# Performance work log

Hardware: AMD Instinct MI355X
Metric: run time of the kernel (lower is better)

Reference implementation:

```python
import jax, jax.numpy as jnp
import numpy as np

B, S, D, U = 32, 2048, 1024, 1024


def setup_inputs() -> dict:
    key = jax.random.key(0)
    ks = jax.random.split(key, 10)
    s = 0.02
    return {
        "dec_hidden": jax.random.normal(ks[0], (B, D), jnp.float32),
        "enc_output": jax.random.normal(ks[1], (B, S, D), jnp.float32),
        "enc_pad_mask": jnp.ones((B, S), jnp.int32),  # accepted but unused, as in the original
        "use_coverage": True,
        "prev_coverage": jax.random.uniform(ks[2], (B, S, 1), jnp.float32),
        "Ws_w": jax.random.normal(ks[3], (D, U), jnp.float32) * s,
        "Ws_b": jnp.zeros((U,), jnp.float32),
        "Wh_w": jax.random.normal(ks[4], (D, U), jnp.float32) * s,
        "Wh_b": jnp.zeros((U,), jnp.float32),
        "Wc_w": jax.random.normal(ks[5], (1, U), jnp.float32) * s,
        "Wc_b": jnp.zeros((U,), jnp.float32),
        "V_w": jax.random.normal(ks[6], (U, 1), jnp.float32) * s,
        "V_b": jnp.zeros((1,), jnp.float32),
    }


def reference(dec_hidden, enc_output, enc_pad_mask, use_coverage, prev_coverage,
              Ws_w, Ws_b, Wh_w, Wh_b, Wc_w, Wc_b, V_w, V_b):
    # W_h(dec_hidden) with time axis: [B, 1, U]
    h = (dec_hidden @ Wh_w + Wh_b)[:, None, :]
    # W_s(enc_output): [B, S, U]
    feat = jnp.einsum('bsd,du->bsu', enc_output, Ws_w) + Ws_b + h
    if use_coverage and prev_coverage is not None:
        # W_c(prev_coverage): [B, S, 1] @ [1, U] -> [B, S, U]
        feat = feat + prev_coverage @ Wc_w + Wc_b
        score = jnp.tanh(feat) @ V_w + V_b            # [B, S, 1]
        attention_weights = jax.nn.softmax(score, axis=1)
        coverage = attention_weights + prev_coverage
    else:
        score = jnp.tanh(feat) @ V_w + V_b
        attention_weights = jax.nn.softmax(score, axis=1)
        coverage = attention_weights if use_coverage else []
    # weighted sum over sequence axis: [B, D]
    context_vector = jnp.sum(attention_weights * enc_output, axis=1)
    return context_vector, jnp.squeeze(attention_weights, -1), coverage
```

## Files before the change

### kernel.cpp

```cpp
#include <hip/hip_runtime.h>
#include <hip/hip_bf16.h>

namespace {

constexpr int kB = 32;
constexpr int kS = 2048;
constexpr int kD = 1024;
constexpr int kU = 1024;

constexpr int BM = 256;
constexpr int BN = 256;
constexpr int kKT = kD / 64;
constexpr int kMT = (kB * kS) / BM;
constexpr int kNT = kU / BN;
constexpr size_t kHalf = 16384;
constexpr size_t kTileChunk = 2 * kHalf;
constexpr size_t kPanel = (size_t)kKT * kTileChunk;

constexpr int kConvBlocks = (kB * kS * kD / 8) / 256;
constexpr int kTpBlocks = (kU / 32) * (kD / 32);
constexpr int kH2Blocks = (kU / 64) * (kB / 4);
constexpr int kPrepBlocks = kConvBlocks + kTpBlocks + kH2Blocks;

typedef __attribute__((ext_vector_type(8))) short bf16x8;
typedef __attribute__((ext_vector_type(4))) float f32x4;

__device__ __forceinline__ unsigned short f2bf(float x) {
  union { __hip_bfloat16 h; unsigned short u; } c;
  c.h = __float2bfloat16(x);
  return c.u;
}

__device__ __forceinline__ float bf2f(unsigned short u) {
  union { unsigned int i; float f; } c;
  c.i = ((unsigned int)u) << 16;
  return c.f;
}

__device__ __forceinline__ float tanh_fast(float x) {
  float e = __expf(2.0f * x);
  return 1.0f - 2.0f * __builtin_amdgcn_rcpf(e + 1.0f);
}

__device__ __forceinline__ void gload16(const void* g, void* l) {
  __builtin_amdgcn_global_load_lds(
      (const __attribute__((address_space(1))) void*)g,
      (__attribute__((address_space(3))) void*)l, 16, 0, 0);
}

#define MFMA_BF16(a, b, c) __builtin_amdgcn_mfma_f32_16x16x32_bf16((a), (b), (c), 0, 0, 0)


__global__ __launch_bounds__(256) void prep_kernel(
    const float* __restrict__ enc, unsigned char* __restrict__ encT,
    const float* __restrict__ Wsw, unsigned char* __restrict__ Bt,
    const float* __restrict__ dec, const float* __restrict__ Whw,
    const float* __restrict__ Whb, const float* __restrict__ Wsb,
    const float* __restrict__ Wcb, float* __restrict__ h2) {
  __shared__ float tile[32][33];
  const int bid = blockIdx.x;
  if (bid < kConvBlocks) {
    const size_t e = ((size_t)bid * 256 + threadIdx.x) * 8;
    const int r = (int)(e >> 10), d0 = (int)(e & 1023);
    float4 v0 = *(const float4*)(enc + e);
    float4 v1 = *(const float4*)(enc + e + 4);
    uint4 p;
    p.x = (unsigned)f2bf(v0.x) | ((unsigned)f2bf(v0.y) << 16);
    p.y = (unsigned)f2bf(v0.z) | ((unsigned)f2bf(v0.w) << 16);
    p.z = (unsigned)f2bf(v1.x) | ((unsigned)f2bf(v1.y) << 16);
    p.w = (unsigned)f2bf(v1.z) | ((unsigned)f2bf(v1.w) << 16);
    const int mt = r >> 8, rh = (r >> 7) & 1, row = r & 127;
    const int kt = d0 >> 6, c8 = (d0 & 63) >> 3;
    unsigned char* dst = encT + (size_t)mt * kPanel + (size_t)kt * kTileChunk +
                         (size_t)rh * kHalf + row * 128 +
                         (((unsigned)c8 << 4) ^ (((unsigned)row & 7) << 4));
    *(uint4*)dst = p;
  } else if (bid < kConvBlocks + kTpBlocks) {
    const int q = bid - kConvBlocks;
    const int u0 = (q & 31) * 32, d0 = (q >> 5) * 32;
    const int tx = threadIdx.x & 31, ty = threadIdx.x >> 5;
    #pragma unroll
    for (int i = 0; i < 4; ++i)
      tile[ty + i * 8][tx] = Wsw[(size_t)(d0 + ty + i * 8) * kU + u0 + tx];
    __syncthreads();
    #pragma unroll
    for (int i = 0; i < 4; ++i) {
      const int u = u0 + ty + i * 8, d = d0 + tx;
      const int nt = u >> 8, gh = (u >> 7) & 1, n = u & 127;
      const int kt = d >> 6, c = d & 63;
      *(unsigned short*)(Bt + (size_t)nt * kPanel + (size_t)kt * kTileChunk +
                         (size_t)gh * kHalf + n * 128 +
                         (((((unsigned)c >> 3) << 4) ^ (((unsigned)n & 7) << 4)) +
                          (c & 7) * 2)) = f2bf(tile[tx][ty + i * 8]);
    }
  } else {
    const int q = bid - kConvBlocks - kTpBlocks;
    const int u = (q & 15) * 64 + (threadIdx.x & 63);
    const int b = (q >> 4) * 4 + (threadIdx.x >> 6);
    float acc = 0.f;
    const float* dh = dec + b * kD;
    #pragma unroll 8
    for (int d = 0; d < kD; ++d) acc += dh[d] * Whw[(size_t)d * kU + u];
    h2[b * kU + u] = acc + Whb[u] + Wsb[u] + Wcb[u];
  }
}

#define READ_A8(AF, ABASE, QR)                                                 \
  _Pragma("unroll")                                                            \
  for (int rfl = 0; rfl < 4; ++rfl) {                                          \
    _Pragma("unroll")                                                          \
    for (int ks = 0; ks < 2; ++ks) {                                           \
      const int row_ = ((QR)*4 + rfl) * 16 + lr;                               \
      AF[rfl][ks] = *(const bf16x8*)((ABASE) + row_ * 128 +                    \
                                     ((ks * 64 + lq * 16) ^ ((lr & 7) << 4))); \
    }                                                                          \
  }

#define READ_B4(BF, BBASE, QC)                                                 \
  _Pragma("unroll")                                                            \
  for (int cfl = 0; cfl < 2; ++cfl) {                                          \
    _Pragma("unroll")                                                          \
    for (int ks = 0; ks < 2; ++ks) {                                           \
      const int row_ = ((QC)*2 + cfl) * 16 + lr;                               \
      BF[cfl][ks] = *(const bf16x8*)((BBASE) + row_ * 128 +                    \
                                     ((ks * 64 + lq * 16) ^ ((lr & 7) << 4))); \
    }                                                                          \
  }

#define MF16(QR, QC, AF, BF)                                                   \
  _Pragma("unroll")                                                            \
  for (int ks = 0; ks < 2; ++ks) {                                             \
    _Pragma("unroll")                                                          \
    for (int rfl = 0; rfl < 4; ++rfl) {                                        \
      _Pragma("unroll")                                                        \
      for (int cfl = 0; cfl < 2; ++cfl)                                        \
        acc[(QR)*4 + rfl][(QC)*2 + cfl] =                                      \
            MFMA_BF16(AF[rfl][ks], BF[cfl][ks], acc[(QR)*4 + rfl][(QC)*2 + cfl]); \
    }                                                                          \
  }

#define STAGE2(GSRC, LDST)                                                     \
  gload16((GSRC) + so0, (LDST) + so0);                                         \
  gload16((GSRC) + so1, (LDST) + so1);

#define FENCE asm volatile("" ::: "memory")
#define BARRIER { FENCE; __builtin_amdgcn_s_barrier(); FENCE; }

__global__ __launch_bounds__(512, 1) void score_gemm4_kernel(
    const unsigned char* __restrict__ encT, const unsigned char* __restrict__ Bt,
    const float* __restrict__ h2, const float* __restrict__ pc,
    const float* __restrict__ Wcw, const float* __restrict__ Vw,
    float* __restrict__ scorep) {
  __shared__ __attribute__((aligned(16))) unsigned char lds[131072];

  const int tid = threadIdx.x;
  const int lane = tid & 63;
  const int w = tid >> 6;
  const int lr = lane & 15, lq = lane >> 4;
  const int wm = w >> 2;
  const int wn = w & 3;
  const int g = wn >> 1;

  const int work = (blockIdx.x & 7) * 128 + (blockIdx.x >> 3);
  const int mtile = work >> 2, ntile = work & 3;

  const unsigned char* Ab = encT + (size_t)mtile * kPanel;
  const unsigned char* Bb = Bt + (size_t)ntile * kPanel;
  const int so0 = tid * 16;
  const int so1 = tid * 16 + 8192;

  unsigned char* Ad0 = lds + (size_t)wm * kHalf;
  unsigned char* Ad1 = lds + (2 + wm) * kHalf;
  unsigned char* Bd0 = lds + 65536 + (size_t)g * kHalf + (wn & 1) * 8192;
  unsigned char* Bd1 = lds + 65536 + (2 + g) * kHalf + (wn & 1) * 8192;
  unsigned char* aSlot[2][2] = {{lds, lds + kHalf}, {lds + 2 * kHalf, lds + 3 * kHalf}};
  unsigned char* bSlot[2][2] = {{lds + 65536, lds + 65536 + kHalf},
                                {lds + 65536 + 2 * kHalf, lds + 65536 + 3 * kHalf}};

  f32x4 acc[8][4];
  #pragma unroll
  for (int i = 0; i < 8; ++i)
    #pragma unroll
    for (int j = 0; j < 4; ++j) acc[i][j] = (f32x4){0.f, 0.f, 0.f, 0.f};

  bf16x8 af[4][2], b0[2][2], b1[2][2];

  STAGE2(Bb, bSlot[0][0]);
  STAGE2(Bb + kHalf, bSlot[0][1]);
  STAGE2(Ab, aSlot[0][0]);
  STAGE2(Ab + kHalf, aSlot[0][1]);
  STAGE2(Bb + kTileChunk, bSlot[1][0]);
  STAGE2(Bb + kTileChunk + kHalf, bSlot[1][1]);
  asm volatile("s_waitcnt vmcnt(4)" ::: "memory");
  BARRIER;

  for (int i = 0; i < kKT / 2; ++i) {
    const int t2 = (i < kKT / 2 - 1) ? 2 * i + 2 : 2 * i;
    const int t3 = (i < kKT / 2 - 1) ? 2 * i + 3 : 2 * i;
    const unsigned char* sA1 = Ab + (size_t)(2 * i + 1) * kTileChunk;
    const unsigned char* sA2 = Ab + (size_t)t2 * kTileChunk;
    const unsigned char* sB2 = Bb + (size_t)t2 * kTileChunk;
    const unsigned char* sB3 = Bb + (size_t)t3 * kTileChunk;

    READ_A8(af, Ad0, 0);
    READ_B4(b0, Bd0, 0);
    STAGE2(sA1, aSlot[1][0]);
    BARRIER;
    __builtin_amdgcn_s_setprio(1);
    MF16(0, 0, af, b0);
    __builtin_amdgcn_s_setprio(0);
    BARRIER;

    READ_B4(b1, Bd0, 1);
    STAGE2(sA1 + kHalf, aSlot[1][1]);
    BARRIER;
    __builtin_amdgcn_s_setprio(1);
    MF16(0, 1, af, b1);
    __builtin_amdgcn_s_setprio(0);
    BARRIER;

    READ_A8(af, Ad0, 1);
    STAGE2(sB2, bSlot[0][0]);
    BARRIER;
    __builtin_amdgcn_s_setprio(1);
    MF16(1, 0, af, b0);
    __builtin_amdgcn_s_setprio(0);
    BARRIER;

    STAGE2(sB2 + kHalf, bSlot[0][1]);
    asm volatile("s_waitcnt vmcnt(4)" ::: "memory");
    BARRIER;
    __builtin_amdgcn_s_setprio(1);
    MF16(1, 1, af, b1);
    __builtin_amdgcn_s_setprio(0);
    BARRIER;

    READ_A8(af, Ad1, 0);
    READ_B4(b0, Bd1, 0);
    STAGE2(sA2, aSlot[0][0]);
    BARRIER;
    __builtin_amdgcn_s_setprio(1);
    MF16(0, 0, af, b0);
    __builtin_amdgcn_s_setprio(0);
    BARRIER;

    READ_B4(b1, Bd1, 1);
    STAGE2(sA2 + kHalf, aSlot[0][1]);
    BARRIER;
    __builtin_amdgcn_s_setprio(1);
    MF16(0, 1, af, b1);
    __builtin_amdgcn_s_setprio(0);
    BARRIER;

    READ_A8(af, Ad1, 1);
    STAGE2(sB3, bSlot[1][0]);
    BARRIER;
    __builtin_amdgcn_s_setprio(1);
    MF16(1, 0, af, b0);
    __builtin_amdgcn_s_setprio(0);
    BARRIER;

    STAGE2(sB3 + kHalf, bSlot[1][1]);
    asm volatile("s_waitcnt vmcnt(4)" ::: "memory");
    BARRIER;
    __builtin_amdgcn_s_setprio(1);
    MF16(1, 1, af, b1);
    __builtin_amdgcn_s_setprio(0);
    BARRIER;
  }
  asm volatile("s_waitcnt vmcnt(0)" ::: "memory");

  const int bidx = mtile >> 3;
  float hv[4], wv[4], vv[4];
  #pragma unroll
  for (int cf = 0; cf < 4; ++cf) {
    const int u = ntile * BN + wn * 64 + cf * 16 + lr;
    hv[cf] = h2[bidx * kU + u];
    wv[cf] = Wcw[u];
    vv[cf] = Vw[u];
  }
  float* plane = scorep + (size_t)(ntile * 4 + wn) * (kB * kS);
  #pragma unroll
  for (int rf = 0; rf < 8; ++rf) {
    #pragma unroll
    for (int j = 0; j < 4; ++j) {
      const int r = mtile * BM + wm * 128 + rf * 16 + lq * 4 + j;
      const float pcv = pc[r];
      float partial = 0.f;
      #pragma unroll
      for (int cf = 0; cf < 4; ++cf) {
        const float feat = acc[rf][cf][j] + hv[cf] + pcv * wv[cf];
        partial += tanh_fast(feat) * vv[cf];
      }
      partial += __shfl_xor(partial, 1);
      partial += __shfl_xor(partial, 2);
      partial += __shfl_xor(partial, 4);
      partial += __shfl_xor(partial, 8);
      if (lr == 0) plane[r] = partial;
    }
  }
}

__global__ __launch_bounds__(256) void softmax2_kernel(
    const float* __restrict__ scorep, const float* __restrict__ pc,
    float* __restrict__ attn, float* __restrict__ cov) {
  const int b = blockIdx.x, tid = threadIdx.x;
  const int lane = tid & 63, wid = tid >> 6;
  const size_t base = (size_t)b * kS + tid * 8;
  float v[8] = {0.f, 0.f, 0.f, 0.f, 0.f, 0.f, 0.f, 0.f};
  #pragma unroll
  for (int p = 0; p < 16; ++p) {
    const float* s = scorep + (size_t)p * (kB * kS) + base;
    float4 a = *(const float4*)(s);
    float4 c = *(const float4*)(s + 4);
    v[0] += a.x; v[1] += a.y; v[2] += a.z; v[3] += a.w;
    v[4] += c.x; v[5] += c.y; v[6] += c.z; v[7] += c.w;
  }
  float m = v[0];
  #pragma unroll
  for (int i = 1; i < 8; ++i) m = fmaxf(m, v[i]);
  #pragma unroll
  for (int msk = 1; msk < 64; msk <<= 1) m = fmaxf(m, __shfl_xor(m, msk));
  __shared__ float redm[4], reds[4];
  if (lane == 0) redm[wid] = m;
  __syncthreads();
  m = fmaxf(fmaxf(redm[0], redm[1]), fmaxf(redm[2], redm[3]));
  float e[8], sum = 0.f;
  #pragma unroll
  for (int i = 0; i < 8; ++i) { e[i] = __expf(v[i] - m); sum += e[i]; }
  #pragma unroll
  for (int msk = 1; msk < 64; msk <<= 1) sum += __shfl_xor(sum, msk);
  if (lane == 0) reds[wid] = sum;
  __syncthreads();
  sum = reds[0] + reds[1] + reds[2] + reds[3];
  const float inv = 1.0f / sum;
  float pv[8], a[8], c[8];
  const float* p = pc + base;
  *(float4*)(pv) = *(const float4*)(p);
  *(float4*)(pv + 4) = *(const float4*)(p + 4);
  #pragma unroll
  for (int i = 0; i < 8; ++i) { a[i] = e[i] * inv; c[i] = a[i] + pv[i]; }
  *(float4*)(attn + base) = *(float4*)(a);
  *(float4*)(attn + base + 4) = *(float4*)(a + 4);
  *(float4*)(cov + base) = *(float4*)(c);
  *(float4*)(cov + base + 4) = *(float4*)(c + 4);
}

__global__ __launch_bounds__(256) void context2_kernel(
    const unsigned char* __restrict__ encT, const float* __restrict__ attn,
    float* __restrict__ ctx) {
  const int kt = blockIdx.x;
  const int b = blockIdx.y;
  const int cg = threadIdx.x & 7;
  const int rgrp = threadIdx.x >> 3;
  float acc8[8];
  #pragma unroll
  for (int j = 0; j < 8; ++j) acc8[j] = 0.f;
  const float* ab = attn + (size_t)b * kS;
  for (int it = 0; it < kS / 32; ++it) {
    const int s = it * 32 + rgrp;
    const int r = b * kS + s;
    const int mt = r >> 8, rh = (r >> 7) & 1, row = r & 127;
    const unsigned char* chunk = encT + (size_t)mt * kPanel +
                                 (size_t)kt * kTileChunk + (size_t)rh * kHalf;
    uint4 v = *(const uint4*)(chunk + row * 128 +
                              ((((unsigned)cg << 4) ^ (((unsigned)row & 7) << 4))));
    const float a = ab[s];
    const unsigned int* vw = (const unsigned int*)&v;
    #pragma unroll
    for (int q = 0; q < 4; ++q) {
      acc8[2 * q]     += a * bf2f((unsigned short)(vw[q] & 0xffff));
      acc8[2 * q + 1] += a * bf2f((unsigned short)(vw[q] >> 16));
    }
  }
  __shared__ float red[256 * 8];
  #pragma unroll
  for (int j = 0; j < 8; ++j) red[threadIdx.x * 8 + j] = acc8[j];
  __syncthreads();
  for (int stride = 16; stride > 0; stride >>= 1) {
    if (rgrp < stride) {
      #pragma unroll
      for (int j = 0; j < 8; ++j)
        red[(rgrp * 8 + cg) * 8 + j] += red[((rgrp + stride) * 8 + cg) * 8 + j];
    }
    __syncthreads();
  }
  if (rgrp == 0) {
    #pragma unroll
    for (int j = 0; j < 8; ++j)
      ctx[(size_t)b * kD + kt * 64 + cg * 8 + j] = red[cg * 8 + j];
  }
}


__global__ __launch_bounds__(256) void h2b_kernel(
    const float* __restrict__ dec, const float* __restrict__ Whw,
    const float* __restrict__ Whb, const float* __restrict__ Wsb,
    const float* __restrict__ Wcb, float* __restrict__ h2) {
  const int u = blockIdx.x * 64 + (threadIdx.x & 63);
  const int b = blockIdx.y * 4 + (threadIdx.x >> 6);
  float acc = 0.f;
  const float* dh = dec + b * kD;
  #pragma unroll 8
  for (int d = 0; d < kD; ++d) acc += dh[d] * Whw[(size_t)d * kU + u];
  h2[b * kU + u] = acc + Whb[u] + Wsb[u] + Wcb[u];
}

__global__ __launch_bounds__(256) void tpose_fb_kernel(
    const float* __restrict__ W, unsigned short* __restrict__ out) {
  __shared__ float tile[32][33];
  const int u0 = blockIdx.x * 32, d0 = blockIdx.y * 32;
  const int tx = threadIdx.x & 31, ty = threadIdx.x >> 5;
  #pragma unroll
  for (int i = 0; i < 4; ++i)
    tile[ty + i * 8][tx] = W[(size_t)(d0 + ty + i * 8) * kU + u0 + tx];
  __syncthreads();
  #pragma unroll
  for (int i = 0; i < 4; ++i)
    out[(size_t)(u0 + ty + i * 8) * kD + d0 + tx] = f2bf(tile[tx][ty + i * 8]);
}

__global__ __launch_bounds__(256, 2) void score_gemm_fb_kernel(
    const float* __restrict__ enc, const unsigned short* __restrict__ WsT,
    const float* __restrict__ h2, const float* __restrict__ pc,
    const float* __restrict__ Wcw, const float* __restrict__ Vw,
    float* __restrict__ score) {
  __shared__ __attribute__((aligned(16))) unsigned char smA[128 * 64 * 2];
  __shared__ __attribute__((aligned(16))) unsigned char smB[128 * 64 * 2];
  const int tid = threadIdx.x;
  const int lane = tid & 63;
  const int wid = tid >> 6;
  const int wr = wid >> 1, wc = wid & 1;
  const int mtile = blockIdx.x >> 3, ntile = blockIdx.x & 7;
  const int r0 = mtile * 128, n0 = ntile * 128;
  f32x4 acc[4][4];
  #pragma unroll
  for (int i = 0; i < 4; ++i)
    #pragma unroll
    for (int j = 0; j < 4; ++j) acc[i][j] = (f32x4){0.f, 0.f, 0.f, 0.f};
  const int kqA = tid & 15;
  const int rowA = tid >> 4;
  const int kcB = tid & 7;
  const int nB = tid >> 3;
  float4 aReg[8];
  uint4 bReg[4];
  #pragma unroll
  for (int i = 0; i < 8; ++i)
    aReg[i] = *(const float4*)(enc + (size_t)(r0 + rowA + 16 * i) * kD + kqA * 4);
  #pragma unroll
  for (int i = 0; i < 4; ++i)
    bReg[i] = *(const uint4*)(WsT + (size_t)(n0 + nB + 32 * i) * kD + kcB * 8);
  const int lr = lane & 15, lq = lane >> 4;
  for (int k0 = 0; k0 < kD; k0 += 64) {
    #pragma unroll
    for (int i = 0; i < 8; ++i) {
      const int row = rowA + 16 * i;
      uint2 p;
      p.x = (unsigned)f2bf(aReg[i].x) | ((unsigned)f2bf(aReg[i].y) << 16);
      p.y = (unsigned)f2bf(aReg[i].z) | ((unsigned)f2bf(aReg[i].w) << 16);
      *(uint2*)(smA + row * 128 + ((kqA * 8) ^ ((row & 7) << 4))) = p;
    }
    #pragma unroll
    for (int i = 0; i < 4; ++i) {
      const int n = nB + 32 * i;
      *(uint4*)(smB + n * 128 + ((kcB * 16) ^ ((n & 7) << 4))) = bReg[i];
    }
    __syncthreads();
    if (k0 + 64 < kD) {
      const int kn = k0 + 64;
      #pragma unroll
      for (int i = 0; i < 8; ++i)
        aReg[i] = *(const float4*)(enc + (size_t)(r0 + rowA + 16 * i) * kD + kn + kqA * 4);
      #pragma unroll
      for (int i = 0; i < 4; ++i)
        bReg[i] = *(const uint4*)(WsT + (size_t)(n0 + nB + 32 * i) * kD + kn + kcB * 8);
    }
    #pragma unroll
    for (int ks = 0; ks < 2; ++ks) {
      const int kb = ks * 64 + lq * 16;
      bf16x8 af2[4], bfr[4];
      #pragma unroll
      for (int fm = 0; fm < 4; ++fm) {
        const int row = wr * 64 + fm * 16 + lr;
        af2[fm] = *(const bf16x8*)(smA + row * 128 + (kb ^ ((row & 7) << 4)));
      }
      #pragma unroll
      for (int fn = 0; fn < 4; ++fn) {
        const int n = wc * 64 + fn * 16 + lr;
        bfr[fn] = *(const bf16x8*)(smB + n * 128 + (kb ^ ((n & 7) << 4)));
      }
      #pragma unroll
      for (int fm = 0; fm < 4; ++fm)
        #pragma unroll
        for (int fn = 0; fn < 4; ++fn)
          acc[fm][fn] = MFMA_BF16(af2[fm], bfr[fn], acc[fm][fn]);
    }
    __syncthreads();
  }
  const int bidx = r0 >> 11;
  float hv[4], wv[4], vv[4];
  #pragma unroll
  for (int fn = 0; fn < 4; ++fn) {
    const int u = n0 + wc * 64 + fn * 16 + lr;
    hv[fn] = h2[bidx * kU + u];
    wv[fn] = Wcw[u];
    vv[fn] = Vw[u];
  }
  #pragma unroll
  for (int fm = 0; fm < 4; ++fm) {
    #pragma unroll
    for (int j = 0; j < 4; ++j) {
      const int r = r0 + wr * 64 + fm * 16 + lq * 4 + j;
      const float pcv = pc[r];
      float partial = 0.f;
      #pragma unroll
      for (int fn = 0; fn < 4; ++fn) {
        const float feat = acc[fm][fn][j] + hv[fn] + pcv * wv[fn];
        partial += tanh_fast(feat) * vv[fn];
      }
      partial += __shfl_xor(partial, 1);
      partial += __shfl_xor(partial, 2);
      partial += __shfl_xor(partial, 4);
      partial += __shfl_xor(partial, 8);
      if (lr == 0) atomicAdd(&score[r], partial);
    }
  }
}

__global__ __launch_bounds__(256) void softmax_fb_kernel(
    const float* __restrict__ score, const float* __restrict__ pc,
    float* __restrict__ attn, float* __restrict__ cov) {
  const int b = blockIdx.x, tid = threadIdx.x;
  const int lane = tid & 63, wid = tid >> 6;
  const float* s = score + (size_t)b * kS;
  float v[8];
  *(float4*)(v) = *(const float4*)(s + tid * 8);
  *(float4*)(v + 4) = *(const float4*)(s + tid * 8 + 4);
  float m = v[0];
  #pragma unroll
  for (int i = 1; i < 8; ++i) m = fmaxf(m, v[i]);
  #pragma unroll
  for (int msk = 1; msk < 64; msk <<= 1) m = fmaxf(m, __shfl_xor(m, msk));
  __shared__ float redm[4], reds[4];
  if (lane == 0) redm[wid] = m;
  __syncthreads();
  m = fmaxf(fmaxf(redm[0], redm[1]), fmaxf(redm[2], redm[3]));
  float e[8], sum = 0.f;
  #pragma unroll
  for (int i = 0; i < 8; ++i) { e[i] = __expf(v[i] - m); sum += e[i]; }
  #pragma unroll
  for (int msk = 1; msk < 64; msk <<= 1) sum += __shfl_xor(sum, msk);
  if (lane == 0) reds[wid] = sum;
  __syncthreads();
  sum = reds[0] + reds[1] + reds[2] + reds[3];
  const float inv = 1.0f / sum;
  float pv[8], a[8], c[8];
  const float* p = pc + (size_t)b * kS + tid * 8;
  *(float4*)(pv) = *(const float4*)(p);
  *(float4*)(pv + 4) = *(const float4*)(p + 4);
  #pragma unroll
  for (int i = 0; i < 8; ++i) { a[i] = e[i] * inv; c[i] = a[i] + pv[i]; }
  *(float4*)(attn + (size_t)b * kS + tid * 8) = *(float4*)(a);
  *(float4*)(attn + (size_t)b * kS + tid * 8 + 4) = *(float4*)(a + 4);
  *(float4*)(cov + (size_t)b * kS + tid * 8) = *(float4*)(c);
  *(float4*)(cov + (size_t)b * kS + tid * 8 + 4) = *(float4*)(c + 4);
}

__global__ __launch_bounds__(256) void context_fb_kernel(
    const float* __restrict__ enc, const float* __restrict__ attn,
    float* __restrict__ ctx) {
  const int b = blockIdx.z;
  const int s0 = blockIdx.y * 256;
  const int d = blockIdx.x * 256 + threadIdx.x;
  const float* e = enc + ((size_t)b * kS + s0) * kD + d;
  const float* a = attn + (size_t)b * kS + s0;
  float acc = 0.f;
  #pragma unroll 8
  for (int s = 0; s < 256; ++s) acc += a[s] * e[(size_t)s * kD];
  atomicAdd(&ctx[b * kD + d], acc);
}

}

extern "C" void kernel_launch(void* const* d_in, const int* in_sizes, int n_in,
                              void* d_out, int out_size, void* d_ws, size_t ws_size,
                              hipStream_t stream) {
  (void)in_sizes; (void)n_in; (void)out_size;
  const float* dec = (const float*)d_in[0];
  const float* enc = (const float*)d_in[1];
  const float* pc  = (const float*)d_in[4];
  const float* Wsw = (const float*)d_in[5];
  const float* Wsb = (const float*)d_in[6];
  const float* Whw = (const float*)d_in[7];
  const float* Whb = (const float*)d_in[8];
  const float* Wcw = (const float*)d_in[9];
  const float* Wcb = (const float*)d_in[10];
  const float* Vw  = (const float*)d_in[11];

  float* ctx  = (float*)d_out;
  float* attn = (float*)d_out + kB * kD;
  float* cov  = attn + kB * kS;

  unsigned char* ws = (unsigned char*)d_ws;

  const size_t encT_sz = (size_t)kB * kS * kD * 2;
  const size_t Bt_sz   = (size_t)kU * kD * 2;
  const size_t h2_sz   = (size_t)kB * kU * 4;
  const size_t sp_sz   = (size_t)16 * kB * kS * 4;
  const size_t need    = encT_sz + Bt_sz + h2_sz + sp_sz;

  if (ws_size >= need) {
    unsigned char* encT = ws;
    unsigned char* Bt   = ws + encT_sz;
    float* h2     = (float*)(ws + encT_sz + Bt_sz);
    float* scorep = (float*)(ws + encT_sz + Bt_sz + h2_sz);

    prep_kernel<<<dim3(kPrepBlocks), 256, 0, stream>>>(
        enc, encT, Wsw, Bt, dec, Whw, Whb, Wsb, Wcb, h2);
    score_gemm4_kernel<<<dim3(kMT * kNT), 512, 0, stream>>>(
        encT, Bt, h2, pc, Wcw, Vw, scorep);
    softmax2_kernel<<<dim3(kB), 256, 0, stream>>>(scorep, pc, attn, cov);
    context2_kernel<<<dim3(kD / 64, kB), 256, 0, stream>>>(encT, attn, ctx);
  } else {
    unsigned short* WsT = (unsigned short*)ws;
    float* h2    = (float*)(ws + (size_t)2 * 1024 * 1024);
    float* score = (float*)(ws + (size_t)2 * 1024 * 1024 + 131072);
    hipMemsetAsync(score, 0, kB * kS * sizeof(float), stream);
    hipMemsetAsync(ctx, 0, kB * kD * sizeof(float), stream);
    h2b_kernel<<<dim3(kU / 64, kB / 4), 256, 0, stream>>>(dec, Whw, Whb, Wsb, Wcb, h2);
    tpose_fb_kernel<<<dim3(kU / 32, kD / 32), 256, 0, stream>>>(Wsw, WsT);
    score_gemm_fb_kernel<<<dim3(4096), 256, 0, stream>>>(
        enc, WsT, h2, pc, Wcw, Vw, score);
    softmax_fb_kernel<<<dim3(kB), 256, 0, stream>>>(score, pc, attn, cov);
    context_fb_kernel<<<dim3(kD / 256, kS / 256, kB), 256, 0, stream>>>(enc, attn, ctx);
  }
}
```

Baseline: 309.7 us.

## Store bf16 encoder in row-major layout and swizzle on GEMM load

The prep kernel now writes the bf16 copy of enc_output in plain row-major order instead of a tiled, pre-swizzled panel layout. It also reorders prep blocks so the h2 and weight-transpose work is dispatched first. The GEMM's A-tile staging computes per-thread row-major source addresses and applies the XOR swizzle on the fly via the global-to-LDS loads. The context kernel reads rows contiguously. The intent is fully coalesced conversion writes and simpler context reads, at the cost of strided 16-byte global reads per row in the GEMM A loads.

```diff
diff --git a/kernel.cpp b/kernel.cpp
--- a/kernel.cpp
+++ b/kernel.cpp
@@ -17,10 +17,10 @@
 constexpr size_t kTileChunk = 2 * kHalf;
 constexpr size_t kPanel = (size_t)kKT * kTileChunk;
 
+constexpr int kH2Blocks = (kU / 64) * (kB / 4);
+constexpr int kTpBlocks = (kU / 32) * (kD / 32);
 constexpr int kConvBlocks = (kB * kS * kD / 8) / 256;
-constexpr int kTpBlocks = (kU / 32) * (kD / 32);
-constexpr int kH2Blocks = (kU / 64) * (kB / 4);
-constexpr int kPrepBlocks = kConvBlocks + kTpBlocks + kH2Blocks;
+constexpr int kPrepBlocks = kH2Blocks + kTpBlocks + kConvBlocks;
 
 typedef __attribute__((ext_vector_type(8))) short bf16x8;
 typedef __attribute__((ext_vector_type(4))) float f32x4;
@@ -52,33 +52,26 @@
 
 
 __global__ __launch_bounds__(256) void prep_kernel(
-    const float* __restrict__ enc, unsigned char* __restrict__ encT,
+    const float* __restrict__ enc, unsigned char* __restrict__ encR,
     const float* __restrict__ Wsw, unsigned char* __restrict__ Bt,
     const float* __restrict__ dec, const float* __restrict__ Whw,
     const float* __restrict__ Whb, const float* __restrict__ Wsb,
     const float* __restrict__ Wcb, float* __restrict__ h2) {
   __shared__ float tile[32][33];
   const int bid = blockIdx.x;
-  if (bid < kConvBlocks) {
-    const size_t e = ((size_t)bid * 256 + threadIdx.x) * 8;
-    const int r = (int)(e >> 10), d0 = (int)(e & 1023);
-    float4 v0 = *(const float4*)(enc + e);
-    float4 v1 = *(const float4*)(enc + e + 4);
-    uint4 p;
-    p.x = (unsigned)f2bf(v0.x) | ((unsigned)f2bf(v0.y) << 16);
-    p.y = (unsigned)f2bf(v0.z) | ((unsigned)f2bf(v0.w) << 16);
-    p.z = (unsigned)f2bf(v1.x) | ((unsigned)f2bf(v1.y) << 16);
-    p.w = (unsigned)f2bf(v1.z) | ((unsigned)f2bf(v1.w) << 16);
-    const int mt = r >> 8, rh = (r >> 7) & 1, row = r & 127;
-    const int kt = d0 >> 6, c8 = (d0 & 63) >> 3;
-    unsigned char* dst = encT + (size_t)mt * kPanel + (size_t)kt * kTileChunk +
-                         (size_t)rh * kHalf + row * 128 +
-                         (((unsigned)c8 << 4) ^ (((unsigned)row & 7) << 4));
-    *(uint4*)dst = p;
-  } else if (bid < kConvBlocks + kTpBlocks) {
-    const int q = bid - kConvBlocks;
+  const int t = threadIdx.x;
+  if (bid < kH2Blocks) {
+    const int u = (bid & 15) * 64 + (t & 63);
+    const int b = (bid >> 4) * 4 + (t >> 6);
+    float acc = 0.f;
+    const float* dh = dec + b * kD;
+    #pragma unroll 8
+    for (int d = 0; d < kD; ++d) acc += dh[d] * Whw[(size_t)d * kU + u];
+    h2[b * kU + u] = acc + Whb[u] + Wsb[u] + Wcb[u];
+  } else if (bid < kH2Blocks + kTpBlocks) {
+    const int q = bid - kH2Blocks;
     const int u0 = (q & 31) * 32, d0 = (q >> 5) * 32;
-    const int tx = threadIdx.x & 31, ty = threadIdx.x >> 5;
+    const int tx = t & 31, ty = t >> 5;
     #pragma unroll
     for (int i = 0; i < 4; ++i)
       tile[ty + i * 8][tx] = Wsw[(size_t)(d0 + ty + i * 8) * kU + u0 + tx];
@@ -94,14 +87,15 @@
                           (c & 7) * 2)) = f2bf(tile[tx][ty + i * 8]);
     }
   } else {
-    const int q = bid - kConvBlocks - kTpBlocks;
-    const int u = (q & 15) * 64 + (threadIdx.x & 63);
-    const int b = (q >> 4) * 4 + (threadIdx.x >> 6);
-    float acc = 0.f;
-    const float* dh = dec + b * kD;
-    #pragma unroll 8
-    for (int d = 0; d < kD; ++d) acc += dh[d] * Whw[(size_t)d * kU + u];
-    h2[b * kU + u] = acc + Whb[u] + Wsb[u] + Wcb[u];
+    const size_t e = ((size_t)(bid - kH2Blocks - kTpBlocks) * 256 + t) * 8;
+    float4 v0 = *(const float4*)(enc + e);
+    float4 v1 = *(const float4*)(enc + e + 4);
+    uint4 p;
+    p.x = (unsigned)f2bf(v0.x) | ((unsigned)f2bf(v0.y) << 16);
+    p.y = (unsigned)f2bf(v0.z) | ((unsigned)f2bf(v0.w) << 16);
+    p.z = (unsigned)f2bf(v1.x) | ((unsigned)f2bf(v1.y) << 16);
+    p.w = (unsigned)f2bf(v1.z) | ((unsigned)f2bf(v1.w) << 16);
+    *(uint4*)(encR + e * 2) = p;
   }
 }
 
@@ -143,11 +137,16 @@
   gload16((GSRC) + so0, (LDST) + so0);                                         \
   gload16((GSRC) + so1, (LDST) + so1);
 
+#define STAGEA(T, H, LDST)                                                     \
+  gload16(Asrc + (size_t)(T) * 128 + (size_t)(H) * 262144, (LDST) + so0);      \
+  gload16(Asrc + (size_t)(T) * 128 + (size_t)(H) * 262144 + 131072,            \
+          (LDST) + so1);
+
 #define FENCE asm volatile("" ::: "memory")
 #define BARRIER { FENCE; __builtin_amdgcn_s_barrier(); FENCE; }
 
 __global__ __launch_bounds__(512, 1) void score_gemm4_kernel(
-    const unsigned char* __restrict__ encT, const unsigned char* __restrict__ Bt,
+    const unsigned char* __restrict__ encR, const unsigned char* __restrict__ Bt,
     const float* __restrict__ h2, const float* __restrict__ pc,
     const float* __restrict__ Wcw, const float* __restrict__ Vw,
     float* __restrict__ scorep) {
@@ -164,7 +163,10 @@
   const int work = (blockIdx.x & 7) * 128 + (blockIdx.x >> 3);
   const int mtile = work >> 2, ntile = work & 3;
 
-  const unsigned char* Ab = encT + (size_t)mtile * kPanel;
+  const int arow = tid >> 3;
+  const unsigned char* Asrc = encR + (size_t)mtile * 524288 +
+                              (size_t)arow * 2048 +
+                              (size_t)(((tid & 7) ^ (arow & 7)) * 16);
   const unsigned char* Bb = Bt + (size_t)ntile * kPanel;
   const int so0 = tid * 16;
   const int so1 = tid * 16 + 8192;
@@ -187,24 +189,23 @@
 
   STAGE2(Bb, bSlot[0][0]);
   STAGE2(Bb + kHalf, bSlot[0][1]);
-  STAGE2(Ab, aSlot[0][0]);
-  STAGE2(Ab + kHalf, aSlot[0][1]);
+  STAGEA(0, 0, aSlot[0][0]);
+  STAGEA(0, 1, aSlot[0][1]);
   STAGE2(Bb + kTileChunk, bSlot[1][0]);
   STAGE2(Bb + kTileChunk + kHalf, bSlot[1][1]);
   asm volatile("s_waitcnt vmcnt(4)" ::: "memory");
   BARRIER;
 
   for (int i = 0; i < kKT / 2; ++i) {
+    const int t1 = 2 * i + 1;
     const int t2 = (i < kKT / 2 - 1) ? 2 * i + 2 : 2 * i;
     const int t3 = (i < kKT / 2 - 1) ? 2 * i + 3 : 2 * i;
-    const unsigned char* sA1 = Ab + (size_t)(2 * i + 1) * kTileChunk;
-    const unsigned char* sA2 = Ab + (size_t)t2 * kTileChunk;
     const unsigned char* sB2 = Bb + (size_t)t2 * kTileChunk;
     const unsigned char* sB3 = Bb + (size_t)t3 * kTileChunk;
 
     READ_A8(af, Ad0, 0);
     READ_B4(b0, Bd0, 0);
-    STAGE2(sA1, aSlot[1][0]);
+    STAGEA(t1, 0, aSlot[1][0]);
     BARRIER;
     __builtin_amdgcn_s_setprio(1);
     MF16(0, 0, af, b0);
@@ -212,7 +213,7 @@
     BARRIER;
 
     READ_B4(b1, Bd0, 1);
-    STAGE2(sA1 + kHalf, aSlot[1][1]);
+    STAGEA(t1, 1, aSlot[1][1]);
     BARRIER;
     __builtin_amdgcn_s_setprio(1);
     MF16(0, 1, af, b1);
@@ -237,7 +238,7 @@
 
     READ_A8(af, Ad1, 0);
     READ_B4(b0, Bd1, 0);
-    STAGE2(sA2, aSlot[0][0]);
+    STAGEA(t2, 0, aSlot[0][0]);
     BARRIER;
     __builtin_amdgcn_s_setprio(1);
     MF16(0, 0, af, b0);
@@ -245,7 +246,7 @@
     BARRIER;
 
     READ_B4(b1, Bd1, 1);
-    STAGE2(sA2 + kHalf, aSlot[0][1]);
+    STAGEA(t2, 1, aSlot[0][1]);
     BARRIER;
     __builtin_amdgcn_s_setprio(1);
     MF16(0, 1, af, b1);
@@ -347,7 +348,7 @@
 }
 
 __global__ __launch_bounds__(256) void context2_kernel(
-    const unsigned char* __restrict__ encT, const float* __restrict__ attn,
+    const unsigned char* __restrict__ encR, const float* __restrict__ attn,
     float* __restrict__ ctx) {
   const int kt = blockIdx.x;
   const int b = blockIdx.y;
@@ -359,12 +360,8 @@
   const float* ab = attn + (size_t)b * kS;
   for (int it = 0; it < kS / 32; ++it) {
     const int s = it * 32 + rgrp;
-    const int r = b * kS + s;
-    const int mt = r >> 8, rh = (r >> 7) & 1, row = r & 127;
-    const unsigned char* chunk = encT + (size_t)mt * kPanel +
-                                 (size_t)kt * kTileChunk + (size_t)rh * kHalf;
-    uint4 v = *(const uint4*)(chunk + row * 128 +
-                              ((((unsigned)cg << 4) ^ (((unsigned)row & 7) << 4))));
+    uint4 v = *(const uint4*)(encR + ((size_t)(b * kS + s)) * 2048 +
+                              kt * 128 + cg * 16);
     const float a = ab[s];
     const unsigned int* vw = (const unsigned int*)&v;
     #pragma unroll
@@ -603,24 +600,24 @@
 
   unsigned char* ws = (unsigned char*)d_ws;
 
-  const size_t encT_sz = (size_t)kB * kS * kD * 2;
+  const size_t encR_sz = (size_t)kB * kS * kD * 2;
   const size_t Bt_sz   = (size_t)kU * kD * 2;
   const size_t h2_sz   = (size_t)kB * kU * 4;
   const size_t sp_sz   = (size_t)16 * kB * kS * 4;
-  const size_t need    = encT_sz + Bt_sz + h2_sz + sp_sz;
+  const size_t need    = encR_sz + Bt_sz + h2_sz + sp_sz;
 
   if (ws_size >= need) {
-    unsigned char* encT = ws;
-    unsigned char* Bt   = ws + encT_sz;
-    float* h2     = (float*)(ws + encT_sz + Bt_sz);
-    float* scorep = (float*)(ws + encT_sz + Bt_sz + h2_sz);
+    unsigned char* encR = ws;
+    unsigned char* Bt   = ws + encR_sz;
+    float* h2     = (float*)(ws + encR_sz + Bt_sz);
+    float* scorep = (float*)(ws + encR_sz + Bt_sz + h2_sz);
 
     prep_kernel<<<dim3(kPrepBlocks), 256, 0, stream>>>(
-        enc, encT, Wsw, Bt, dec, Whw, Whb, Wsb, Wcb, h2);
+        enc, encR, Wsw, Bt, dec, Whw, Whb, Wsb, Wcb, h2);
     score_gemm4_kernel<<<dim3(kMT * kNT), 512, 0, stream>>>(
-        encT, Bt, h2, pc, Wcw, Vw, scorep);
+        encR, Bt, h2, pc, Wcw, Vw, scorep);
     softmax2_kernel<<<dim3(kB), 256, 0, stream>>>(scorep, pc, attn, cov);
-    context2_kernel<<<dim3(kD / 64, kB), 256, 0, stream>>>(encT, attn, ctx);
+    context2_kernel<<<dim3(kD / 64, kB), 256, 0, stream>>>(encR, attn, ctx);
   } else {
     unsigned short* WsT = (unsigned short*)ws;
     float* h2    = (float*)(ws + (size_t)2 * 1024 * 1024);
```

Measured after the change: 291.4 us. 5.9% less time.
